# Kernel tuning notes

Measured on AMD Instinct MI355X. Metric: run time of the kernel, lower is better.

Reference implementation:

```python
import jax, jax.numpy as jnp
import numpy as np

IN_CHN, OUT_CHN, K = 64, 64, 3
STRIDE, PADDING = 1, 1


def setup_inputs() -> dict:
    key = jax.random.key(0)
    k1, k2 = jax.random.split(key)
    Activation = jax.random.normal(k1, (32, IN_CHN, 112, 112), dtype=jnp.float32)
    weights = jax.random.uniform(k2, (IN_CHN * OUT_CHN * K * K, 1), dtype=jnp.float32) * 0.001
    return {"Activation": Activation, "weights": weights}


def _binarize_ste(x):
    # sign(x) in forward, identity gradient (straight-through estimator)
    return x + jax.lax.stop_gradient(jnp.sign(x) - x)


def reference(Activation, weights):
    real_weights = weights.reshape(OUT_CHN, IN_CHN, K, K)
    bin_act = _binarize_ste(Activation)      # [N, C, H, W], values in {-1, 0, 1}
    bin_w = _binarize_ste(real_weights)      # [O, I, K, K]
    out = jax.lax.conv_general_dilated(
        bin_act, bin_w,
        window_strides=(STRIDE, STRIDE),
        padding=[(PADDING, PADDING), (PADDING, PADDING)],
        dimension_numbers=("NCHW", "OIHW", "NCHW"),
    )
    return out
```

## Files before the change

### kernel.cpp

```cpp
#include <hip/hip_runtime.h>
#include <stdint.h>


#define NN 32
#define CC 64
#define HH 112
#define WW 112
#define OO 64
#define HW (HH*WW)
#define NHW (NN*HW)

typedef float  vfloat4 __attribute__((ext_vector_type(4)));
typedef float  vfloat2 __attribute__((ext_vector_type(2)));

#define PACK_BLOCK 256
#define PACK_A_BLOCKS (NHW/4/PACK_BLOCK)

#define INT_GPR 54
#define INT_ROWS 110
#define INT_GPI (INT_GPR*INT_ROWS)
#define INT_THREADS (NN*INT_GPI)
#define INT_BLOCKS ((INT_THREADS+255)/256)

#define BOR_PPI 664
#define BOR_THREADS (NN*BOR_PPI)
#define BOR_BLOCKS (BOR_THREADS/256)

#define CONV_BLOCKS (BOR_BLOCKS + INT_BLOCKS)

__global__ __launch_bounds__(PACK_BLOCK)
void pack_kernel(const float* __restrict__ act, const float* __restrict__ wgt,
                 uint64_t* __restrict__ ap, uint64_t* __restrict__ wp) {
    int b = blockIdx.x;
    if (b == PACK_A_BLOCKS) {
        for (int t = threadIdx.x; t < OO * 9; t += PACK_BLOCK) {
            int o = t / 9, k = t - o * 9;
            uint32_t lo = 0, hi = 0;
            #pragma unroll
            for (int i = 0; i < 64; ++i) {
                uint32_t s = __float_as_uint(wgt[(o * 64 + i) * 9 + k]) >> 31;
                if (i < 32) lo |= s << i;
                else        hi |= s << (i - 32);
            }
            wp[t] = ((uint64_t)hi << 32) | lo;
        }
        return;
    }
    int t = b * PACK_BLOCK + threadIdx.x;
    int n = t / (HW / 4);
    int rem4 = t - n * (HW / 4);
    const vfloat4* base = (const vfloat4*)act + (size_t)n * CC * (HW / 4) + rem4;
    uint32_t lo[4] = {0, 0, 0, 0}, hi[4] = {0, 0, 0, 0};
    #pragma unroll
    for (int c = 0; c < 64; ++c) {
        vfloat4 v = __builtin_nontemporal_load(base + (size_t)c * (HW / 4));
        uint32_t s0 = __float_as_uint(v.x) >> 31;
        uint32_t s1 = __float_as_uint(v.y) >> 31;
        uint32_t s2 = __float_as_uint(v.z) >> 31;
        uint32_t s3 = __float_as_uint(v.w) >> 31;
        if (c < 32) {
            lo[0] |= s0 << c; lo[1] |= s1 << c; lo[2] |= s2 << c; lo[3] |= s3 << c;
        } else {
            int cc = c - 32;
            hi[0] |= s0 << cc; hi[1] |= s1 << cc; hi[2] |= s2 << cc; hi[3] |= s3 << cc;
        }
    }
    ulonglong2 w01, w23;
    w01.x = ((uint64_t)hi[0] << 32) | lo[0];
    w01.y = ((uint64_t)hi[1] << 32) | lo[1];
    w23.x = ((uint64_t)hi[2] << 32) | lo[2];
    w23.y = ((uint64_t)hi[3] << 32) | lo[3];
    ulonglong2* dst = (ulonglong2*)(ap + (size_t)t * 4);
    dst[0] = w01;
    dst[1] = w23;
}

__global__ __launch_bounds__(256)
void conv_kernel(const uint64_t* __restrict__ ap, const uint64_t* __restrict__ wp,
                 float* __restrict__ out) {
    if (blockIdx.x >= BOR_BLOCKS) {
        int t = (blockIdx.x - BOR_BLOCKS) * 256 + threadIdx.x;
        if (t >= INT_THREADS) return;
        int n = t / INT_GPI;
        int rem = t - n * INT_GPI;
        int hr = rem / INT_GPR;
        int gw = rem - hr * INT_GPR;
        int h = hr + 1;
        int w0 = 2 + 2 * gw;
        const uint64_t* apn = ap + (size_t)n * HW + (h - 1) * WW + (w0 - 1);
        uint64_t a[3][4];
        #pragma unroll
        for (int r = 0; r < 3; ++r)
            #pragma unroll
            for (int c = 0; c < 4; ++c)
                a[r][c] = apn[r * WW + c];
        float* op = out + (size_t)n * (OO * HW) + h * WW + w0;
        for (int o = 0; o < OO; ++o) {
            const uint64_t* wk = wp + o * 9;
            int s0 = 0, s1 = 0;
            #pragma unroll
            for (int r = 0; r < 3; ++r)
                #pragma unroll
                for (int c = 0; c < 3; ++c) {
                    uint64_t w = wk[r * 3 + c];
                    s0 += __popcll(a[r][c]     ^ w);
                    s1 += __popcll(a[r][c + 1] ^ w);
                }
            vfloat2 v = {(float)(576 - 2 * s0), (float)(576 - 2 * s1)};
            __builtin_nontemporal_store(v, (vfloat2*)(op + (size_t)o * HW));
        }
        return;
    }
    int t = blockIdx.x * 256 + threadIdx.x;
    int n = t / BOR_PPI;
    int b = t - n * BOR_PPI;
    int h, w;
    if (b < 112)      { h = 0;   w = b; }
    else if (b < 224) { h = 111; w = b - 112; }
    else {
        int c = b - 224;
        h = 1 + (c >> 2);
        int q = c & 3;
        w = q + ((q >= 2) ? 108 : 0);
    }
    const uint64_t* apn = ap + (size_t)n * HW;
    uint64_t a[9], m[9];
    int nvalid = 0;
    #pragma unroll
    for (int kh = 0; kh < 3; ++kh) {
        int hh = h + kh - 1;
        bool hv = (unsigned)hh < (unsigned)HH;
        #pragma unroll
        for (int kw = 0; kw < 3; ++kw) {
            int ww2 = w + kw - 1;
            bool wv = (unsigned)ww2 < (unsigned)WW;
            bool v = hv && wv;
            int k = kh * 3 + kw;
            int ch = hv ? hh : h;
            int cw = wv ? ww2 : w;
            a[k] = apn[ch * WW + cw];
            m[k] = v ? ~0ull : 0ull;
            nvalid += v ? 1 : 0;
        }
    }
    int base = 64 * nvalid;
    float* op = out + (size_t)n * (OO * HW) + h * WW + w;
    for (int o = 0; o < OO; ++o) {
        const uint64_t* wk = wp + o * 9;
        int s = 0;
        #pragma unroll
        for (int k = 0; k < 9; ++k)
            s += __popcll((a[k] ^ wk[k]) & m[k]);
        __builtin_nontemporal_store((float)(base - 2 * s), op + (size_t)o * HW);
    }
}

extern "C" void kernel_launch(void* const* d_in, const int* in_sizes, int n_in,
                              void* d_out, int out_size, void* d_ws, size_t ws_size,
                              hipStream_t stream) {
    const float* act = (const float*)d_in[0];
    const float* wgt = (const float*)d_in[1];
    float* out = (float*)d_out;

    uint64_t* wp = (uint64_t*)d_ws;
    uint64_t* ap = wp + 1024;

    pack_kernel<<<PACK_A_BLOCKS + 1, PACK_BLOCK, 0, stream>>>(act, wgt, ap, wp);
    conv_kernel<<<CONV_BLOCKS, 256, 0, stream>>>(ap, wp, out);
}
```

Before: 230.7 us.

## Split output channels across four thread groups and use regular stores

Each conv thread now handles 16 output channels instead of 64, and the grid grows fourfold with the output-channel group index taken as wave-uniform via readfirstlane. This raises parallelism and shortens each thread's serial loop, at the cost of loading and packing the activation neighbourhood four times. Output stores also switch from nontemporal to plain stores.

```diff
diff --git a/kernel.cpp b/kernel.cpp
--- a/kernel.cpp
+++ b/kernel.cpp
@@ -11,19 +11,23 @@
 #define NHW (NN*HW)
 
 typedef float  vfloat4 __attribute__((ext_vector_type(4)));
-typedef float  vfloat2 __attribute__((ext_vector_type(2)));
 
 #define PACK_BLOCK 256
 #define PACK_A_BLOCKS (NHW/4/PACK_BLOCK)
 
+#define OG  4
+#define OPG 16
+
 #define INT_GPR 54
 #define INT_ROWS 110
 #define INT_GPI (INT_GPR*INT_ROWS)
-#define INT_THREADS (NN*INT_GPI)
-#define INT_BLOCKS ((INT_THREADS+255)/256)
+#define INT_PAIRS (NN*INT_GPI)
+#define INT_THREADS (INT_PAIRS*OG)
+#define INT_BLOCKS (INT_THREADS/256)
 
 #define BOR_PPI 664
-#define BOR_THREADS (NN*BOR_PPI)
+#define BOR_TOT (NN*BOR_PPI)
+#define BOR_THREADS (BOR_TOT*OG)
 #define BOR_BLOCKS (BOR_THREADS/256)
 
 #define CONV_BLOCKS (BOR_BLOCKS + INT_BLOCKS)
@@ -80,9 +84,10 @@
                  float* __restrict__ out) {
     if (blockIdx.x >= BOR_BLOCKS) {
         int t = (blockIdx.x - BOR_BLOCKS) * 256 + threadIdx.x;
-        if (t >= INT_THREADS) return;
-        int n = t / INT_GPI;
-        int rem = t - n * INT_GPI;
+        int og = __builtin_amdgcn_readfirstlane(t / INT_PAIRS);
+        int r = t - og * INT_PAIRS;
+        int n = r / INT_GPI;
+        int rem = r - n * INT_GPI;
         int hr = rem / INT_GPR;
         int gw = rem - hr * INT_GPR;
         int h = hr + 1;
@@ -90,30 +95,33 @@
         const uint64_t* apn = ap + (size_t)n * HW + (h - 1) * WW + (w0 - 1);
         uint64_t a[3][4];
         #pragma unroll
-        for (int r = 0; r < 3; ++r)
+        for (int rr = 0; rr < 3; ++rr)
             #pragma unroll
             for (int c = 0; c < 4; ++c)
-                a[r][c] = apn[r * WW + c];
-        float* op = out + (size_t)n * (OO * HW) + h * WW + w0;
-        for (int o = 0; o < OO; ++o) {
-            const uint64_t* wk = wp + o * 9;
+                a[rr][c] = apn[rr * WW + c];
+        float* op = out + (size_t)n * (OO * HW) + (size_t)(og * OPG) * HW + h * WW + w0;
+        const uint64_t* wbase = wp + og * (OPG * 9);
+        for (int oo = 0; oo < OPG; ++oo) {
+            const uint64_t* wk = wbase + oo * 9;
             int s0 = 0, s1 = 0;
             #pragma unroll
-            for (int r = 0; r < 3; ++r)
+            for (int rr = 0; rr < 3; ++rr)
                 #pragma unroll
                 for (int c = 0; c < 3; ++c) {
-                    uint64_t w = wk[r * 3 + c];
-                    s0 += __popcll(a[r][c]     ^ w);
-                    s1 += __popcll(a[r][c + 1] ^ w);
+                    uint64_t w = wk[rr * 3 + c];
+                    s0 += __popcll(a[rr][c]     ^ w);
+                    s1 += __popcll(a[rr][c + 1] ^ w);
                 }
-            vfloat2 v = {(float)(576 - 2 * s0), (float)(576 - 2 * s1)};
-            __builtin_nontemporal_store(v, (vfloat2*)(op + (size_t)o * HW));
+            float2 v = make_float2((float)(576 - 2 * s0), (float)(576 - 2 * s1));
+            *(float2*)(op + (size_t)oo * HW) = v;
         }
         return;
     }
     int t = blockIdx.x * 256 + threadIdx.x;
-    int n = t / BOR_PPI;
-    int b = t - n * BOR_PPI;
+    int og = __builtin_amdgcn_readfirstlane(t / BOR_TOT);
+    int r = t - og * BOR_TOT;
+    int n = r / BOR_PPI;
+    int b = r - n * BOR_PPI;
     int h, w;
     if (b < 112)      { h = 0;   w = b; }
     else if (b < 224) { h = 111; w = b - 112; }
@@ -144,14 +152,15 @@
         }
     }
     int base = 64 * nvalid;
-    float* op = out + (size_t)n * (OO * HW) + h * WW + w;
-    for (int o = 0; o < OO; ++o) {
-        const uint64_t* wk = wp + o * 9;
+    float* op = out + (size_t)n * (OO * HW) + (size_t)(og * OPG) * HW + h * WW + w;
+    const uint64_t* wbase = wp + og * (OPG * 9);
+    for (int oo = 0; oo < OPG; ++oo) {
+        const uint64_t* wk = wbase + oo * 9;
         int s = 0;
         #pragma unroll
         for (int k = 0; k < 9; ++k)
             s += __popcll((a[k] ^ wk[k]) & m[k]);
-        __builtin_nontemporal_store((float)(base - 2 * s), op + (size_t)o * HW);
+        op[(size_t)oo * HW] = (float)(base - 2 * s);
     }
 }
 
```

Result: faster. 221.1 us (-4.1%).
